# Kernel tuning notes

Measured on AMD Instinct MI355X. Metric: run time of the kernel, lower is better.

## Reference

```python
import jax, jax.numpy as jnp
import numpy as np

N_NODES = 100000
N_EDGES = 1600000
D_FEAT = 128
HIDDEN = 16
N_CLASSES = 16


def setup_inputs() -> dict:
    key = jax.random.key(0)
    ks = jax.random.split(key, 6)
    x = jax.random.normal(ks[0], (N_NODES, D_FEAT), dtype=jnp.float32)
    edge_index = jax.random.randint(ks[1], (2, N_EDGES), 0, N_NODES, dtype=jnp.int64)
    # Glorot-ish scaled weights
    w1_rel = jax.random.normal(ks[2], (D_FEAT, HIDDEN), dtype=jnp.float32) / np.sqrt(D_FEAT)
    w1_root = jax.random.normal(ks[3], (D_FEAT, HIDDEN), dtype=jnp.float32) / np.sqrt(D_FEAT)
    b1 = jnp.zeros((HIDDEN,), dtype=jnp.float32)
    w2_rel = jax.random.normal(ks[4], (HIDDEN, N_CLASSES), dtype=jnp.float32) / np.sqrt(HIDDEN)
    w2_root = jax.random.normal(ks[5], (HIDDEN, N_CLASSES), dtype=jnp.float32) / np.sqrt(HIDDEN)
    b2 = jnp.zeros((N_CLASSES,), dtype=jnp.float32)
    return {"x": x, "edge_index": edge_index, "w1_rel": w1_rel, "w1_root": w1_root,
            "b1": b1, "w2_rel": w2_rel, "w2_root": w2_root, "b2": b2}


def _graph_conv(x, src, dst, w_rel, w_root, b):
    # PyG GraphConv(aggr='add'): out_i = lin_rel(sum_{j->i} x_j) + lin_root(x_i)
    n = x.shape[0]
    agg = jax.ops.segment_sum(x[src], dst, num_segments=n)  # [N, d_in]
    return agg @ w_rel + x @ w_root + b


def reference(x, edge_index, w1_rel, w1_root, b1, w2_rel, w2_root, b2):
    src, dst = edge_index[0], edge_index[1]
    h = jax.nn.relu(_graph_conv(x, src, dst, w1_rel, w1_root, b1))
    # F.dropout(training=False) -> identity in eval mode
    out = _graph_conv(h, src, dst, w2_rel, w2_root, b2)
    return jax.nn.log_softmax(out, axis=1)
```

## Files before the change

kernel.cpp:

```cpp
#include <hip/hip_runtime.h>

#define DFEAT 128
#define HID 16
#define BKT_NODES 128
#define BKT_SHIFT 7
#define CAP 2432
#define CAPI 10
#define CHUNK 4096
#define NOEDGE 0xFFFFFFFFu

typedef __attribute__((ext_vector_type(8))) short short8;
typedef __attribute__((ext_vector_type(4))) float floatx4;

__device__ __forceinline__ float bf2f(unsigned v) { return __uint_as_float(v << 16); }
__device__ __forceinline__ unsigned short f2bf(float f) {
    unsigned u = __float_as_uint(f);
    return (unsigned short)((u + 0x7FFFu + ((u >> 16) & 1u)) >> 16);
}
__device__ __forceinline__ unsigned pack2(float a, float b) {
    return (unsigned)f2bf(a) | ((unsigned)f2bf(b) << 16);
}

__global__ __launch_bounds__(512) void k_detect(const unsigned short* __restrict__ x,
                                                const int* __restrict__ ei,
                                                int* __restrict__ flags,
                                                int* __restrict__ gcur, int nbkt) {
    const int t = threadIdx.x;
    for (int i = t; i < nbkt; i += 512) gcur[i] = 0;
    if (t < 64) {
        unsigned short v = x[2 * t];
        int e = (v >> 7) & 0xFF;
        bool okbf = (v == 0) || (e >= 110 && e <= 130);
        unsigned long long mbf = __ballot(okbf);
        bool z = (ei[2 * t + 1] == 0);
        unsigned long long mz = __ballot(z);
        if (t == 0) {
            flags[0] = (__popcll(mbf) >= 52) ? 1 : 0;
            flags[1] = (__popcll(mz) >= 60) ? 1 : 0;
        }
    }
}

__global__ __launch_bounds__(256) void k_part(const int* __restrict__ ei,
                                              unsigned* __restrict__ eb,
                                              int* __restrict__ gcur,
                                              const int* __restrict__ flags,
                                              int E, int nbkt) {
    __shared__ int hist[1024];
    const int t = threadIdx.x;
    for (int i = t; i < nbkt; i += 256) hist[i] = 0;
    __syncthreads();
    const int base = blockIdx.x * CHUNK;
    const int i64 = flags[1];
    unsigned pk[16];
    unsigned short bk[16];
#pragma unroll
    for (int i = 0; i < 16; ++i) {
        int e = base + i * 256 + t;
        if (e < E) {
            int src, dst;
            if (i64) { src = ei[2 * (size_t)e]; dst = ei[2 * ((size_t)E + e)]; }
            else     { src = ei[e];             dst = ei[(size_t)E + e]; }
            int b = dst >> BKT_SHIFT;
            pk[i] = ((unsigned)src << BKT_SHIFT) | (unsigned)(dst & (BKT_NODES - 1));
            bk[i] = (unsigned short)b;
            atomicAdd(&hist[b], 1);
        } else {
            bk[i] = 0xFFFFu;
        }
    }
    __syncthreads();
    for (int b = t; b < nbkt; b += 256) {
        int c = hist[b];
        hist[b] = c ? atomicAdd(&gcur[b], c) : 0;
    }
    __syncthreads();
#pragma unroll
    for (int i = 0; i < 16; ++i) {
        if (bk[i] != 0xFFFFu) {
            int pos = atomicAdd(&hist[bk[i]], 1);
            if (pos >= 0 && pos < CAP)
                eb[(size_t)bk[i] * CAP + pos] = pk[i];
        }
    }
}

__global__ __launch_bounds__(256) void k_lin1(const void* __restrict__ xv,
                                              const void* __restrict__ wrel,
                                              const void* __restrict__ wroot,
                                              unsigned short* __restrict__ p1b,
                                              unsigned short* __restrict__ q1b,
                                              const int* __restrict__ flags,
                                              int N) {
    const int t = threadIdx.x;
    const int lane = t & 63, wave = t >> 6;
    const int bf = flags[0];
    const int m = lane & 15;
    const int quad = lane >> 4;
    const int nodebase = blockIdx.x * 64 + wave * 16;

    short8 Brel[4], Broot[4];
    if (bf) {
        const unsigned short* a = (const unsigned short*)wrel;
        const unsigned short* c = (const unsigned short*)wroot;
#pragma unroll
        for (int kb = 0; kb < 4; ++kb) {
            short8 br, bo;
#pragma unroll
            for (int j = 0; j < 8; ++j) {
                int k = kb * 32 + quad * 8 + j;
                br[j] = (short)a[k * HID + m];
                bo[j] = (short)c[k * HID + m];
            }
            Brel[kb] = br; Broot[kb] = bo;
        }
    } else {
        const float* a = (const float*)wrel;
        const float* c = (const float*)wroot;
#pragma unroll
        for (int kb = 0; kb < 4; ++kb) {
            short8 br, bo;
#pragma unroll
            for (int j = 0; j < 8; ++j) {
                int k = kb * 32 + quad * 8 + j;
                br[j] = (short)f2bf(a[k * HID + m]);
                bo[j] = (short)f2bf(c[k * HID + m]);
            }
            Brel[kb] = br; Broot[kb] = bo;
        }
    }

    int row = nodebase + m;
    if (row >= N) row = N - 1;

    floatx4 accP = {0.f, 0.f, 0.f, 0.f}, accQ = {0.f, 0.f, 0.f, 0.f};
    if (bf) {
        const unsigned short* xp = (const unsigned short*)xv;
        const unsigned short* rp = xp + (size_t)row * DFEAT + quad * 8;
#pragma unroll
        for (int kb = 0; kb < 4; ++kb) {
            short8 A = *(const short8*)(rp + kb * 32);
            accP = __builtin_amdgcn_mfma_f32_16x16x32_bf16(A, Brel[kb], accP, 0, 0, 0);
            accQ = __builtin_amdgcn_mfma_f32_16x16x32_bf16(A, Broot[kb], accQ, 0, 0, 0);
        }
    } else {
        const float* xp = (const float*)xv;
        const float* rp = xp + (size_t)row * DFEAT + quad * 8;
#pragma unroll
        for (int kb = 0; kb < 4; ++kb) {
            float4 v0 = *(const float4*)(rp + kb * 32);
            float4 v1 = *(const float4*)(rp + kb * 32 + 4);
            short8 A;
            A[0] = (short)f2bf(v0.x); A[1] = (short)f2bf(v0.y);
            A[2] = (short)f2bf(v0.z); A[3] = (short)f2bf(v0.w);
            A[4] = (short)f2bf(v1.x); A[5] = (short)f2bf(v1.y);
            A[6] = (short)f2bf(v1.z); A[7] = (short)f2bf(v1.w);
            accP = __builtin_amdgcn_mfma_f32_16x16x32_bf16(A, Brel[kb], accP, 0, 0, 0);
            accQ = __builtin_amdgcn_mfma_f32_16x16x32_bf16(A, Broot[kb], accQ, 0, 0, 0);
        }
    }

#pragma unroll
    for (int r = 0; r < 4; ++r) {
        int node = nodebase + quad * 4 + r;
        if (node < N) {
            p1b[(size_t)node * HID + m] = f2bf(accP[r]);
            q1b[(size_t)node * HID + m] = f2bf(accQ[r]);
        }
    }
}

__global__ __launch_bounds__(256) void k_sagg1(const unsigned* __restrict__ eb,
                                               const int* __restrict__ gcur,
                                               const unsigned short* __restrict__ p1b,
                                               const unsigned short* __restrict__ q1b,
                                               const void* __restrict__ b1,
                                               const void* __restrict__ w2rel,
                                               const void* __restrict__ w2root,
                                               unsigned short* __restrict__ p2b,
                                               unsigned short* __restrict__ q2b,
                                               unsigned* __restrict__ csr,
                                               int* __restrict__ offsets,
                                               int* __restrict__ ends,
                                               const int* __restrict__ flags,
                                               int N) {
    __shared__ unsigned srt[CAP];
    __shared__ int cnts[BKT_NODES];
    __shared__ int offs[BKT_NODES];
    __shared__ float4 swp[HID][8];
    __shared__ float sb[HID];
    const int t = threadIdx.x;
    const int b = blockIdx.x;
    const int bf = flags[0];

    if (t < 128) {
        int k = t >> 3, p = t & 7;
        float4 w;
        if (bf) {
            const unsigned short* a = (const unsigned short*)w2rel;
            const unsigned short* c = (const unsigned short*)w2root;
            w = make_float4(bf2f(a[k * 16 + 2 * p]), bf2f(a[k * 16 + 2 * p + 1]),
                            bf2f(c[k * 16 + 2 * p]), bf2f(c[k * 16 + 2 * p + 1]));
        } else {
            const float* a = (const float*)w2rel;
            const float* c = (const float*)w2root;
            w = make_float4(a[k * 16 + 2 * p], a[k * 16 + 2 * p + 1],
                            c[k * 16 + 2 * p], c[k * 16 + 2 * p + 1]);
        }
        swp[k][p] = w;
    }
    if (t < HID) sb[t] = bf ? bf2f(((const unsigned short*)b1)[t]) : ((const float*)b1)[t];
    if (t < BKT_NODES) cnts[t] = 0;
    __syncthreads();

    int cnt = gcur[b];
    if (cnt < 0) cnt = 0;
    if (cnt > CAP) cnt = CAP;
    const unsigned* ep = eb + (size_t)b * CAP;

    unsigned ev[CAPI];
    int rk[CAPI];
#pragma unroll
    for (int i = 0; i < CAPI; ++i) {
        int e = i * 256 + t;
        if (e < cnt) {
            unsigned w = ep[e];
            ev[i] = w;
            rk[i] = atomicAdd(&cnts[w & (BKT_NODES - 1u)], 1);
        } else ev[i] = NOEDGE;
    }
    __syncthreads();
    if (t < BKT_NODES) offs[t] = cnts[t];
    __syncthreads();
    for (int off = 1; off < BKT_NODES; off <<= 1) {
        int v = 0;
        if (t >= off && t < BKT_NODES) v = offs[t - off];
        __syncthreads();
        if (t < BKT_NODES) offs[t] += v;
        __syncthreads();
    }
#pragma unroll
    for (int i = 0; i < CAPI; ++i) {
        if (ev[i] != NOEDGE) {
            unsigned local = ev[i] & (BKT_NODES - 1u);
            int pos = offs[local] - cnts[local] + rk[i];
            srt[pos] = ev[i] >> BKT_SHIFT;
        }
    }
    __syncthreads();

    const int base = b * CAP;
    for (int e = t; e < cnt; e += 256) csr[base + e] = srt[e];
    const int gb = b * BKT_NODES;
    if (t < BKT_NODES) {
        int gn = gb + t;
        if (gn < N) {
            offsets[gn] = base + offs[t] - cnts[t];
            ends[gn]    = base + offs[t];
        }
    }

    const int grp = t >> 3, jp = t & 7;
#pragma unroll
    for (int g = 0; g < 4; ++g) {
        int node = g * 32 + grp;
        int gn = gb + node;
        int beg = offs[node] - cnts[node];
        int end = offs[node];
        float2 acc = make_float2(0.f, 0.f);
        int e = beg;
        for (; e + 4 <= end; e += 4) {
            unsigned s0 = srt[e], s1 = srt[e + 1], s2 = srt[e + 2], s3 = srt[e + 3];
            unsigned u0 = *(const unsigned*)(p1b + (size_t)s0 * HID + 2 * jp);
            unsigned u1 = *(const unsigned*)(p1b + (size_t)s1 * HID + 2 * jp);
            unsigned u2 = *(const unsigned*)(p1b + (size_t)s2 * HID + 2 * jp);
            unsigned u3 = *(const unsigned*)(p1b + (size_t)s3 * HID + 2 * jp);
            acc.x += bf2f(u0 & 0xFFFFu) + bf2f(u1 & 0xFFFFu)
                   + bf2f(u2 & 0xFFFFu) + bf2f(u3 & 0xFFFFu);
            acc.y += bf2f(u0 >> 16) + bf2f(u1 >> 16) + bf2f(u2 >> 16) + bf2f(u3 >> 16);
        }
        for (; e < end; ++e) {
            unsigned u = *(const unsigned*)(p1b + (size_t)srt[e] * HID + 2 * jp);
            acc.x += bf2f(u & 0xFFFFu);
            acc.y += bf2f(u >> 16);
        }
        float hx = 0.f, hy = 0.f;
        if (gn < N) {
            unsigned qu = *(const unsigned*)(q1b + (size_t)gn * HID + 2 * jp);
            hx = fmaxf(acc.x + bf2f(qu & 0xFFFFu) + sb[2 * jp], 0.f);
            hy = fmaxf(acc.y + bf2f(qu >> 16) + sb[2 * jp + 1], 0.f);
        }
        float2 sp = make_float2(0.f, 0.f), sq = make_float2(0.f, 0.f);
#pragma unroll
        for (int k = 0; k < HID; ++k) {
            float hsel = (k & 1) ? hy : hx;
            float hk = __shfl(hsel, k >> 1, 8);
            float4 w = swp[k][jp];
            sp.x += hk * w.x; sp.y += hk * w.y;
            sq.x += hk * w.z; sq.y += hk * w.w;
        }
        if (gn < N) {
            ((unsigned*)p2b)[(size_t)gn * 8 + jp] = pack2(sp.x, sp.y);
            ((unsigned*)q2b)[(size_t)gn * 8 + jp] = pack2(sq.x, sq.y);
        }
    }
}

__global__ __launch_bounds__(256) void k_agg2(const int* __restrict__ offsets,
                                              const int* __restrict__ ends,
                                              const unsigned* __restrict__ csr,
                                              const unsigned short* __restrict__ p2b,
                                              const unsigned short* __restrict__ q2b,
                                              const void* __restrict__ b2,
                                              void* __restrict__ out,
                                              const int* __restrict__ flags,
                                              int N) {
    __shared__ float sb[HID];
    const int t = threadIdx.x;
    const int bf = flags[0];
    if (t < HID) sb[t] = bf ? bf2f(((const unsigned short*)b2)[t]) : ((const float*)b2)[t];
    __syncthreads();

    const int grp = t >> 3, jp = t & 7;
    const int n = blockIdx.x * 32 + grp;
    if (n >= N) return;

    const int beg = offsets[n], end = ends[n];
    float2 acc = make_float2(0.f, 0.f);
    int e = beg;
    for (; e + 8 <= end; e += 8) {
        unsigned s0 = csr[e],     s1 = csr[e + 1], s2 = csr[e + 2], s3 = csr[e + 3];
        unsigned s4 = csr[e + 4], s5 = csr[e + 5], s6 = csr[e + 6], s7 = csr[e + 7];
        unsigned u0 = *(const unsigned*)(p2b + (size_t)s0 * HID + 2 * jp);
        unsigned u1 = *(const unsigned*)(p2b + (size_t)s1 * HID + 2 * jp);
        unsigned u2 = *(const unsigned*)(p2b + (size_t)s2 * HID + 2 * jp);
        unsigned u3 = *(const unsigned*)(p2b + (size_t)s3 * HID + 2 * jp);
        unsigned u4 = *(const unsigned*)(p2b + (size_t)s4 * HID + 2 * jp);
        unsigned u5 = *(const unsigned*)(p2b + (size_t)s5 * HID + 2 * jp);
        unsigned u6 = *(const unsigned*)(p2b + (size_t)s6 * HID + 2 * jp);
        unsigned u7 = *(const unsigned*)(p2b + (size_t)s7 * HID + 2 * jp);
        acc.x += bf2f(u0 & 0xFFFFu) + bf2f(u1 & 0xFFFFu)
               + bf2f(u2 & 0xFFFFu) + bf2f(u3 & 0xFFFFu)
               + bf2f(u4 & 0xFFFFu) + bf2f(u5 & 0xFFFFu)
               + bf2f(u6 & 0xFFFFu) + bf2f(u7 & 0xFFFFu);
        acc.y += bf2f(u0 >> 16) + bf2f(u1 >> 16) + bf2f(u2 >> 16) + bf2f(u3 >> 16)
               + bf2f(u4 >> 16) + bf2f(u5 >> 16) + bf2f(u6 >> 16) + bf2f(u7 >> 16);
    }
    for (; e + 2 <= end; e += 2) {
        unsigned s0 = csr[e], s1 = csr[e + 1];
        unsigned u0 = *(const unsigned*)(p2b + (size_t)s0 * HID + 2 * jp);
        unsigned u1 = *(const unsigned*)(p2b + (size_t)s1 * HID + 2 * jp);
        acc.x += bf2f(u0 & 0xFFFFu) + bf2f(u1 & 0xFFFFu);
        acc.y += bf2f(u0 >> 16) + bf2f(u1 >> 16);
    }
    for (; e < end; ++e) {
        unsigned u = *(const unsigned*)(p2b + (size_t)csr[e] * HID + 2 * jp);
        acc.x += bf2f(u & 0xFFFFu);
        acc.y += bf2f(u >> 16);
    }
    unsigned qu = *(const unsigned*)(q2b + (size_t)n * HID + 2 * jp);
    float ox = acc.x + bf2f(qu & 0xFFFFu) + sb[2 * jp];
    float oy = acc.y + bf2f(qu >> 16) + sb[2 * jp + 1];

    float m = fmaxf(ox, oy);
#pragma unroll
    for (int mask = 1; mask < 8; mask <<= 1) m = fmaxf(m, __shfl_xor(m, mask, 8));
    float s = __expf(ox - m) + __expf(oy - m);
#pragma unroll
    for (int mask = 1; mask < 8; mask <<= 1) s += __shfl_xor(s, mask, 8);
    const float l = m + __logf(s);

    if (bf) ((unsigned*)out)[(size_t)n * 8 + jp] = pack2(ox - l, oy - l);
    else    ((float2*)out)[(size_t)n * 8 + jp] = make_float2(ox - l, oy - l);
}

extern "C" void kernel_launch(void* const* d_in, const int* in_sizes, int n_in,
                              void* d_out, int out_size, void* d_ws, size_t ws_size,
                              hipStream_t stream) {
    const void* x       = d_in[0];
    const int*  ei      = (const int*)d_in[1];
    const void* w1_rel  = d_in[2];
    const void* w1_root = d_in[3];
    const void* b1      = d_in[4];
    const void* w2_rel  = d_in[5];
    const void* w2_root = d_in[6];
    const void* b2      = d_in[7];

    const int N = in_sizes[0] / DFEAT;
    const int E = in_sizes[1] / 2;
    const int nbkt = (N + BKT_NODES - 1) / BKT_NODES;

    unsigned short* p1b = (unsigned short*)d_ws;
    unsigned short* q1b = p1b + (size_t)N * HID;
    unsigned short* p2b = q1b + (size_t)N * HID;
    unsigned short* q2b = p2b + (size_t)N * HID;
    unsigned* eb   = (unsigned*)(q2b + (size_t)N * HID);
    unsigned* csr  = eb + (size_t)nbkt * CAP;
    int* offsets   = (int*)(csr + (size_t)nbkt * CAP);
    int* ends      = offsets + N;
    int* gcur      = ends + N;
    int* flags     = gcur + nbkt;

    k_detect<<<1, 512, 0, stream>>>((const unsigned short*)x, ei, flags, gcur, nbkt);
    k_part<<<(E + CHUNK - 1) / CHUNK, 256, 0, stream>>>(ei, eb, gcur, flags, E, nbkt);
    k_lin1<<<(N + 63) / 64, 256, 0, stream>>>(x, w1_rel, w1_root, p1b, q1b, flags, N);
    k_sagg1<<<nbkt, 256, 0, stream>>>(eb, gcur, p1b, q1b, b1, w2_rel, w2_root,
                                      p2b, q2b, csr, offsets, ends, flags, N);
    k_agg2<<<(N + 31) / 32, 256, 0, stream>>>(offsets, ends, csr, p2b, q2b, b2,
                                              d_out, flags, N);
}
```

Measured before the change: 177.1 us.

## Merge edge partition and first linear layer into one launch with vectorized int64 edge loads

After: 164.5 us. 1.08x faster.

```diff
diff --git a/kernel.cpp b/kernel.cpp
--- a/kernel.cpp
+++ b/kernel.cpp
@@ -41,63 +41,85 @@
     }
 }
 
-__global__ __launch_bounds__(256) void k_part(const int* __restrict__ ei,
-                                              unsigned* __restrict__ eb,
-                                              int* __restrict__ gcur,
-                                              const int* __restrict__ flags,
-                                              int E, int nbkt) {
+__global__ __launch_bounds__(256) void k_pl(const int* __restrict__ ei,
+                                            unsigned* __restrict__ eb,
+                                            int* __restrict__ gcur,
+                                            const void* __restrict__ xv,
+                                            const void* __restrict__ wrel,
+                                            const void* __restrict__ wroot,
+                                            unsigned short* __restrict__ p1b,
+                                            unsigned short* __restrict__ q1b,
+                                            const int* __restrict__ flags,
+                                            int E, int nbkt, int N, int nPart) {
     __shared__ int hist[1024];
     const int t = threadIdx.x;
-    for (int i = t; i < nbkt; i += 256) hist[i] = 0;
-    __syncthreads();
-    const int base = blockIdx.x * CHUNK;
-    const int i64 = flags[1];
-    unsigned pk[16];
-    unsigned short bk[16];
-#pragma unroll
-    for (int i = 0; i < 16; ++i) {
-        int e = base + i * 256 + t;
-        if (e < E) {
-            int src, dst;
-            if (i64) { src = ei[2 * (size_t)e]; dst = ei[2 * ((size_t)E + e)]; }
-            else     { src = ei[e];             dst = ei[(size_t)E + e]; }
-            int b = dst >> BKT_SHIFT;
-            pk[i] = ((unsigned)src << BKT_SHIFT) | (unsigned)(dst & (BKT_NODES - 1));
-            bk[i] = (unsigned short)b;
-            atomicAdd(&hist[b], 1);
+
+    if ((int)blockIdx.x < nPart) {
+        for (int i = t; i < nbkt; i += 256) hist[i] = 0;
+        __syncthreads();
+        const int base = blockIdx.x * CHUNK;
+        const int i64 = flags[1];
+        unsigned pk[16];
+        unsigned short bk[16];
+        if (i64 && !(E & 1)) {
+#pragma unroll
+            for (int ip = 0; ip < 8; ++ip) {
+                int e = base + ip * 512 + 2 * t;
+                if (e < E) {
+                    int4 sv = *(const int4*)(ei + 2 * (size_t)e);
+                    int4 dv = *(const int4*)(ei + 2 * ((size_t)E + e));
+                    int b0 = dv.x >> BKT_SHIFT;
+                    pk[2 * ip] = ((unsigned)sv.x << BKT_SHIFT) | (unsigned)(dv.x & (BKT_NODES - 1));
+                    bk[2 * ip] = (unsigned short)b0;
+                    atomicAdd(&hist[b0], 1);
+                    int b1 = dv.z >> BKT_SHIFT;
+                    pk[2 * ip + 1] = ((unsigned)sv.z << BKT_SHIFT) | (unsigned)(dv.z & (BKT_NODES - 1));
+                    bk[2 * ip + 1] = (unsigned short)b1;
+                    atomicAdd(&hist[b1], 1);
+                } else {
+                    bk[2 * ip] = 0xFFFFu;
+                    bk[2 * ip + 1] = 0xFFFFu;
+                }
+            }
         } else {
-            bk[i] = 0xFFFFu;
-        }
-    }
-    __syncthreads();
-    for (int b = t; b < nbkt; b += 256) {
-        int c = hist[b];
-        hist[b] = c ? atomicAdd(&gcur[b], c) : 0;
-    }
-    __syncthreads();
-#pragma unroll
-    for (int i = 0; i < 16; ++i) {
-        if (bk[i] != 0xFFFFu) {
-            int pos = atomicAdd(&hist[bk[i]], 1);
-            if (pos >= 0 && pos < CAP)
-                eb[(size_t)bk[i] * CAP + pos] = pk[i];
-        }
-    }
-}
-
-__global__ __launch_bounds__(256) void k_lin1(const void* __restrict__ xv,
-                                              const void* __restrict__ wrel,
-                                              const void* __restrict__ wroot,
-                                              unsigned short* __restrict__ p1b,
-                                              unsigned short* __restrict__ q1b,
-                                              const int* __restrict__ flags,
-                                              int N) {
-    const int t = threadIdx.x;
+#pragma unroll
+            for (int i = 0; i < 16; ++i) {
+                int e = base + i * 256 + t;
+                if (e < E) {
+                    int src, dst;
+                    if (i64) { src = ei[2 * (size_t)e]; dst = ei[2 * ((size_t)E + e)]; }
+                    else     { src = ei[e];             dst = ei[(size_t)E + e]; }
+                    int b = dst >> BKT_SHIFT;
+                    pk[i] = ((unsigned)src << BKT_SHIFT) | (unsigned)(dst & (BKT_NODES - 1));
+                    bk[i] = (unsigned short)b;
+                    atomicAdd(&hist[b], 1);
+                } else {
+                    bk[i] = 0xFFFFu;
+                }
+            }
+        }
+        __syncthreads();
+        for (int b = t; b < nbkt; b += 256) {
+            int c = hist[b];
+            hist[b] = c ? atomicAdd(&gcur[b], c) : 0;
+        }
+        __syncthreads();
+#pragma unroll
+        for (int i = 0; i < 16; ++i) {
+            if (bk[i] != 0xFFFFu) {
+                int pos = atomicAdd(&hist[bk[i]], 1);
+                if (pos >= 0 && pos < CAP)
+                    eb[(size_t)bk[i] * CAP + pos] = pk[i];
+            }
+        }
+        return;
+    }
+
     const int lane = t & 63, wave = t >> 6;
     const int bf = flags[0];
     const int m = lane & 15;
     const int quad = lane >> 4;
-    const int nodebase = blockIdx.x * 64 + wave * 16;
+    const int nodebase = ((int)blockIdx.x - nPart) * 64 + wave * 16;
 
     short8 Brel[4], Broot[4];
     if (bf) {
@@ -401,9 +423,12 @@
     int* gcur      = ends + N;
     int* flags     = gcur + nbkt;
 
+    const int nPart = (E + CHUNK - 1) / CHUNK;
+    const int nLin  = (N + 63) / 64;
+
     k_detect<<<1, 512, 0, stream>>>((const unsigned short*)x, ei, flags, gcur, nbkt);
-    k_part<<<(E + CHUNK - 1) / CHUNK, 256, 0, stream>>>(ei, eb, gcur, flags, E, nbkt);
-    k_lin1<<<(N + 63) / 64, 256, 0, stream>>>(x, w1_rel, w1_root, p1b, q1b, flags, N);
+    k_pl<<<nPart + nLin, 256, 0, stream>>>(ei, eb, gcur, x, w1_rel, w1_root,
+                                           p1b, q1b, flags, E, nbkt, N, nPart);
     k_sagg1<<<nbkt, 256, 0, stream>>>(eb, gcur, p1b, q1b, b1, w2_rel, w2_root,
                                       p2b, q2b, csr, offsets, ends, flags, N);
     k_agg2<<<(N + 31) / 32, 256, 0, stream>>>(offsets, ends, csr, p2b, q2b, b2,
```
